# Optimization experiments

Hardware: AMD Instinct MI355X
Metric: run time of the kernel (lower is better)

## Reference

```python
import jax, jax.numpy as jnp
import numpy as np

D_MODEL = 128
N_HEADS = 4
HEAD_DIM = D_MODEL // N_HEADS
NUM_NODES = 64
L = 4096
B = 2


def build_st_causal_mask(seq_len, num_nodes):
    t = seq_len // num_nodes
    time_mask = jnp.tril(jnp.ones((t, t), dtype=bool))  # [T, T]
    # expand to [T, N, T, N] -> [L, L]; attend to all nodes at same/earlier time
    m = jnp.broadcast_to(time_mask[:, None, :, None], (t, num_nodes, t, num_nodes))
    return m.reshape(seq_len, seq_len)


def setup_inputs() -> dict:
    key = jax.random.key(0)
    ks = jax.random.split(key, 12)
    q = jax.random.normal(ks[0], (L, B, D_MODEL), dtype=jnp.float32)
    # xavier-uniform-ish init scales
    lim = np.sqrt(6.0 / (D_MODEL + D_MODEL)) / np.sqrt(2.0)
    W_Q = jax.random.uniform(ks[3], (D_MODEL, D_MODEL), minval=-lim, maxval=lim)
    W_K = jax.random.uniform(ks[4], (D_MODEL, D_MODEL), minval=-lim, maxval=lim)
    W_V = jax.random.uniform(ks[5], (D_MODEL, D_MODEL), minval=-lim, maxval=lim)
    lim_o = np.sqrt(6.0 / (D_MODEL + D_MODEL))
    W_O = jax.random.uniform(ks[6], (D_MODEL, D_MODEL), minval=-lim_o, maxval=lim_o)
    b_Q = jnp.zeros((D_MODEL,), jnp.float32)
    b_K = jnp.zeros((D_MODEL,), jnp.float32)
    b_V = jnp.zeros((D_MODEL,), jnp.float32)
    b_O = jnp.zeros((D_MODEL,), jnp.float32)
    return {
        "query": q,
        "key": jax.random.normal(ks[1], (L, B, D_MODEL), dtype=jnp.float32),
        "value": jax.random.normal(ks[2], (L, B, D_MODEL), dtype=jnp.float32),
        "W_Q": W_Q, "b_Q": b_Q, "W_K": W_K, "b_K": b_K,
        "W_V": W_V, "b_V": b_V, "W_O": W_O, "b_O": b_O,
    }


def reference(query, key, value, W_Q, b_Q, W_K, b_K, W_V, b_V, W_O, b_O):
    Lq, Bq, C = query.shape
    scaling = HEAD_DIM ** (-0.5)
    # torch Linear: x @ W.T + b
    q = (query @ W_Q.T + b_Q) * scaling
    k = key @ W_K.T + b_K
    v = value @ W_V.T + b_V
    # [L, B, C] -> [B, H, L, Dh]
    def split_heads(x):
        return x.reshape(Lq, Bq, N_HEADS, HEAD_DIM).transpose(1, 2, 0, 3)
    q, k, v = split_heads(q), split_heads(k), split_heads(v)
    scores = jnp.einsum("bhqd,bhkd->bhqk", q, k)  # [B, H, L, L]
    mask = build_st_causal_mask(Lq, NUM_NODES)  # [L, L] bool
    scores = jnp.where(mask[None, None], scores, -jnp.inf)
    attn = jax.nn.softmax(scores, axis=-1)
    context = jnp.einsum("bhqk,bhkd->bhqd", attn, v)  # [B, H, L, Dh]
    context = context.transpose(0, 2, 1, 3).reshape(Bq, Lq, C)  # [B, L, C]
    out = context @ W_O.T + b_O  # [B, L, C]
    return out
```

## Files before the change

kernel.cpp:

```cpp
#include <hip/hip_runtime.h>

#define L_SEQ 4096
#define BATCH 2
#define NHEAD 4
#define DHEAD 32
#define DMODEL 128

typedef __attribute__((ext_vector_type(4))) float floatx4;
typedef __attribute__((ext_vector_type(16))) float floatx16;
typedef __attribute__((ext_vector_type(8))) __bf16 bf16x8;
typedef __attribute__((ext_vector_type(8))) unsigned short ushort8;
typedef __attribute__((ext_vector_type(4))) unsigned int uintx4;

__device__ __forceinline__ floatx4 MFMA(ushort8 a, ushort8 b, floatx4 c) {
  return __builtin_amdgcn_mfma_f32_16x16x32_bf16(
      __builtin_bit_cast(bf16x8, a), __builtin_bit_cast(bf16x8, b), c, 0, 0, 0);
}
__device__ __forceinline__ floatx16 MFMA32(ushort8 a, ushort8 b, floatx16 c) {
  return __builtin_amdgcn_mfma_f32_32x32x16_bf16(
      __builtin_bit_cast(bf16x8, a), __builtin_bit_cast(bf16x8, b), c, 0, 0, 0);
}

__device__ __forceinline__ unsigned short f2bf(float f) {
  union { float f; unsigned int u; } x; x.f = f;
  unsigned int u = x.u + 0x7fffu + ((x.u >> 16) & 1u);
  return (unsigned short)(u >> 16);
}

__device__ __forceinline__ unsigned pkbf(float lo, float hi) {
  unsigned r;
  asm("v_cvt_pk_bf16_f32 %0, %1, %2" : "=v"(r) : "v"(lo), "v"(hi));
  return r;
}

#define WLDS 136

__global__ __launch_bounds__(256) void proj_kernel(
    const float* __restrict__ xq, const float* __restrict__ xk,
    const float* __restrict__ xv,
    const float* __restrict__ WQ, const float* __restrict__ bQ,
    const float* __restrict__ WK, const float* __restrict__ bK,
    const float* __restrict__ WV, const float* __restrict__ bV,
    unsigned short* __restrict__ Qs, unsigned short* __restrict__ Ks,
    unsigned short* __restrict__ Vt)
{
  __shared__ unsigned short Wl[128 * WLDS];
  __shared__ float bl[128];
  const int mat = blockIdx.z;
  const int b   = blockIdx.y;
  const int l0  = blockIdx.x * 64;
  const float* __restrict__ x    = (mat == 0) ? xq : (mat == 1) ? xk : xv;
  const float* __restrict__ W    = (mat == 0) ? WQ : (mat == 1) ? WK : WV;
  const float* __restrict__ bias = (mat == 0) ? bQ : (mat == 1) ? bK : bV;
  const int tid = threadIdx.x;

  #pragma unroll
  for (int it = 0; it < 16; ++it) {
    int idx = tid + it * 256;
    int row = idx >> 5;
    int col = (idx & 31) * 4;
    floatx4 v = *(const floatx4*)(W + row * 128 + col);
    unsigned short* dst = Wl + row * WLDS + col;
    dst[0] = f2bf(v[0]); dst[1] = f2bf(v[1]);
    dst[2] = f2bf(v[2]); dst[3] = f2bf(v[3]);
  }
  if (tid < 128) bl[tid] = bias[tid];
  __syncthreads();

  const int w = tid >> 6, lane = tid & 63;
  const int g = lane >> 4, qi = lane & 15;

  ushort8 xf[4];
  #pragma unroll
  for (int kk = 0; kk < 4; ++kk) {
    const float* src = x + ((size_t)(l0 + w * 16 + qi) * BATCH + b) * DMODEL + kk * 32 + g * 8;
    floatx4 a = *(const floatx4*)src;
    floatx4 c = *(const floatx4*)(src + 4);
    ushort8 f;
    f[0]=f2bf(a[0]); f[1]=f2bf(a[1]); f[2]=f2bf(a[2]); f[3]=f2bf(a[3]);
    f[4]=f2bf(c[0]); f[5]=f2bf(c[1]); f[6]=f2bf(c[2]); f[7]=f2bf(c[3]);
    xf[kk] = f;
  }

  floatx4 acc[8];
  #pragma unroll
  for (int n = 0; n < 8; ++n) acc[n] = (floatx4){0.f, 0.f, 0.f, 0.f};

  #pragma unroll
  for (int kk = 0; kk < 4; ++kk) {
    #pragma unroll
    for (int n = 0; n < 8; ++n) {
      ushort8 wf = *(const ushort8*)(Wl + (n * 16 + qi) * WLDS + kk * 32 + g * 8);
      acc[n] = (mat == 2) ? MFMA(wf, xf[kk], acc[n]) : MFMA(xf[kk], wf, acc[n]);
    }
  }

  const int hb4 = b * NHEAD;
  if (mat == 0) {
    const float scale = 0.17677669529663687f;
    #pragma unroll
    for (int n = 0; n < 8; ++n) {
      int c = n * 16 + qi;
      int h = c >> 5, dh = c & 31;
      float bb = bl[c];
      #pragma unroll
      for (int r = 0; r < 4; ++r) {
        int lq = l0 + w * 16 + 4 * g + r;
        float v = (acc[n][r] + bb) * scale;
        Qs[((size_t)(hb4 + h) * L_SEQ + lq) * DHEAD + dh] = f2bf(v);
      }
    }
  } else if (mat == 1) {
    #pragma unroll
    for (int n = 0; n < 8; ++n) {
      int c = n * 16 + qi;
      int h = c >> 5, dh = c & 31;
      int dj  = (dh >> 4) & 1;
      int hi2 = (dh >> 3) & 1;
      int e   = dh & 7;
      float bb = bl[c];
      #pragma unroll
      for (int r = 0; r < 4; ++r) {
        int lq = l0 + w * 16 + 4 * g + r;
        int t   = lq >> 6;
        int rr  = lq & 63;
        int ql2 = rr & 31, rhi = rr >> 5;
        size_t off = ((((size_t)(hb4 + h) * 64 + t) * 4 + (2 * rhi + dj)) * 64
                      + (hi2 * 32 + ql2)) * 8 + e;
        Ks[off] = f2bf(acc[n][r] + bb);
      }
    }
  } else {
    #pragma unroll
    for (int n = 0; n < 8; ++n) {
      #pragma unroll
      for (int r = 0; r < 4; ++r) {
        int cout = n * 16 + 4 * g + r;
        int h = cout >> 5, dh2 = cout & 31;
        float v = acc[n][r] + bl[cout];
        int lq  = l0 + w * 16 + qi;
        int t   = lq >> 6;
        int kvt = lq & 63;
        int s   = kvt >> 4;
        int u   = kvt & 15;
        int b2  = (u >> 3) & 1;
        int hi2 = (u >> 2) & 1;
        int e2  = u & 3;
        size_t off = ((((size_t)(hb4 + h) * 64 + t) * 4 + s) * 64
                      + (hi2 * 32 + dh2)) * 8 + (4 * b2 + e2);
        Vt[off] = f2bf(v);
      }
    }
  }
}

__global__ __launch_bounds__(256, 4) void attn_kernel(
    const unsigned short* __restrict__ Qs, const unsigned short* __restrict__ Ks,
    const unsigned short* __restrict__ Vt,
    float* __restrict__ Opart, float* __restrict__ MLpart)
{
  __shared__ float Tr[4][32 * 36];

  const int tid = threadIdx.x;
  const int w = tid >> 6, lane = tid & 63;
  const int ql = lane & 31, hi = lane >> 5;

  const int ph    = blockIdx.x;
  const int plane = ph >> 1;
  const int half  = ph & 1;
  const int j     = blockIdx.y;
  const int bq    = j & 15, mq = j >> 4;
  const int tq    = (mq == 0) ? bq : (mq == 1) ? 63 - bq
                  : (mq == 2) ? 16 + bq : 47 - bq;

  const int c     = w;
  const int width = (tq >> 2) + 1;
  const int t0    = c * width;
  const int tend  = min(t0 + width, tq + 1);

  const unsigned short* __restrict__ Qh = Qs + (size_t)plane * L_SEQ * DHEAD;

  const int q0 = tq * 64 + half * 32;
  ushort8 qf0 = *(const ushort8*)(Qh + (size_t)(q0 + ql) * DHEAD + hi * 8);
  ushort8 qf1 = *(const ushort8*)(Qh + (size_t)(q0 + ql) * DHEAD + 16 + hi * 8);

  const floatx16 z16 = {0,0,0,0,0,0,0,0,0,0,0,0,0,0,0,0};
  floatx16 acc_a = z16, acc_b = z16;
  float m = -1e30f, l = 0.f;

  const unsigned short* kb = Ks + ((size_t)plane * 64 + t0) * 2048 + (size_t)lane * 8;
  const unsigned short* vb = Vt + ((size_t)plane * 64 + t0) * 2048 + (size_t)lane * 8;

  #pragma unroll 2
  for (int t = t0; t < tend; ++t) {
    ushort8 kf00 = *(const ushort8*)(kb);
    ushort8 kf01 = *(const ushort8*)(kb + 512);
    ushort8 kf10 = *(const ushort8*)(kb + 1024);
    ushort8 kf11 = *(const ushort8*)(kb + 1536);
    ushort8 va0  = *(const ushort8*)(vb);
    ushort8 va1  = *(const ushort8*)(vb + 512);
    ushort8 va2  = *(const ushort8*)(vb + 1024);
    ushort8 va3  = *(const ushort8*)(vb + 1536);
    kb += 2048;
    vb += 2048;

    floatx16 St0 = MFMA32(kf00, qf0, z16);
    St0 = MFMA32(kf01, qf1, St0);
    floatx16 St1 = MFMA32(kf10, qf0, z16);
    St1 = MFMA32(kf11, qf1, St1);

    float pmax = St0[0];
    #pragma unroll
    for (int i = 1; i < 16; ++i) pmax = fmaxf(pmax, St0[i]);
    #pragma unroll
    for (int i = 0; i < 16; ++i) pmax = fmaxf(pmax, St1[i]);
    pmax = fmaxf(pmax, __shfl_xor(pmax, 32));

    if (__any(pmax > m + 8.0f)) {
      float mnew = fmaxf(m, pmax);
      float corr = __expf(m - mnew);
      m = mnew;
      l *= corr;
      #pragma unroll
      for (int i = 0; i < 16; ++i) { acc_a[i] *= corr; acc_b[i] *= corr; }
    }
    float rsum = 0.f;
    #pragma unroll
    for (int i = 0; i < 16; ++i) { float e = __expf(St0[i] - m); St0[i] = e; rsum += e; }
    #pragma unroll
    for (int i = 0; i < 16; ++i) { float e = __expf(St1[i] - m); St1[i] = e; rsum += e; }
    rsum += __shfl_xor(rsum, 32);
    l += rsum;

    uintx4 pb;
    pb[0] = pkbf(St0[0], St0[1]); pb[1] = pkbf(St0[2], St0[3]);
    pb[2] = pkbf(St0[4], St0[5]); pb[3] = pkbf(St0[6], St0[7]);
    acc_a = MFMA32(va0, __builtin_bit_cast(ushort8, pb), acc_a);
    pb[0] = pkbf(St0[8], St0[9]);  pb[1] = pkbf(St0[10], St0[11]);
    pb[2] = pkbf(St0[12], St0[13]); pb[3] = pkbf(St0[14], St0[15]);
    acc_a = MFMA32(va1, __builtin_bit_cast(ushort8, pb), acc_a);
    pb[0] = pkbf(St1[0], St1[1]); pb[1] = pkbf(St1[2], St1[3]);
    pb[2] = pkbf(St1[4], St1[5]); pb[3] = pkbf(St1[6], St1[7]);
    acc_b = MFMA32(va2, __builtin_bit_cast(ushort8, pb), acc_b);
    pb[0] = pkbf(St1[8], St1[9]);  pb[1] = pkbf(St1[10], St1[11]);
    pb[2] = pkbf(St1[12], St1[13]); pb[3] = pkbf(St1[14], St1[15]);
    acc_b = MFMA32(va3, __builtin_bit_cast(ushort8, pb), acc_b);
  }

  const int slot = ((plane * 64 + tq) * 4 + c);
  float* T = &Tr[w][0];
  #pragma unroll
  for (int r = 0; r < 16; ++r) {
    int dh = (r & 3) + 8 * (r >> 2) + 4 * hi;
    T[ql * 36 + dh] = acc_a[r] + acc_b[r];
  }
  asm volatile("s_waitcnt lgkmcnt(0)" ::: "memory");
  __builtin_amdgcn_sched_barrier(0);

  const int qr = lane >> 1, dg = (lane & 1) * 16;
  float* __restrict__ Op = Opart + (size_t)slot * 2048 + half * 32 * 32;
  #pragma unroll
  for (int j2 = 0; j2 < 4; ++j2) {
    floatx4 vv = *(const floatx4*)(T + qr * 36 + dg + 4 * j2);
    *(floatx4*)(Op + qr * 32 + dg + 4 * j2) = vv;
  }
  if (hi == 0) {
    MLpart[(size_t)slot * 128 + (half * 32 + ql) * 2 + 0] = m;
    MLpart[(size_t)slot * 128 + (half * 32 + ql) * 2 + 1] = l;
  }
}

__global__ __launch_bounds__(256) void combine_kernel(
    const float* __restrict__ Opart, const float* __restrict__ MLpart,
    unsigned short* __restrict__ ctx)
{
  const int tq = blockIdx.x;
  const int hb = blockIdx.y;
  const int tid = threadIdx.x;
  const int q  = tid >> 2;
  const int dg = tid & 3;
  const int slot0 = (hb * 64 + tq) * 4;

  float mv[4], lv[4];
  float M = -1e30f;
  #pragma unroll
  for (int ci = 0; ci < 4; ++ci) {
    mv[ci] = MLpart[(size_t)(slot0 + ci) * 128 + q * 2 + 0];
    lv[ci] = MLpart[(size_t)(slot0 + ci) * 128 + q * 2 + 1];
    M = fmaxf(M, mv[ci]);
  }
  float Lsum = 0.f;
  float wgt[4];
  #pragma unroll
  for (int ci = 0; ci < 4; ++ci) {
    wgt[ci] = __expf(mv[ci] - M);
    Lsum += wgt[ci] * lv[ci];
  }
  float inv = 1.0f / Lsum;

  floatx4 a0 = (floatx4){0.f,0.f,0.f,0.f}, a1 = (floatx4){0.f,0.f,0.f,0.f};
  #pragma unroll
  for (int ci = 0; ci < 4; ++ci) {
    const float* Op = Opart + (size_t)(slot0 + ci) * 2048 + q * 32 + dg * 8;
    floatx4 o0 = *(const floatx4*)(Op);
    floatx4 o1 = *(const floatx4*)(Op + 4);
    float wv = wgt[ci];
    a0 += wv * o0;
    a1 += wv * o1;
  }
  const int b = hb >> 2, hh = hb & 3;
  size_t base = ((size_t)b * L_SEQ + tq * 64 + q) * DMODEL + hh * 32 + dg * 8;
  #pragma unroll
  for (int j = 0; j < 4; ++j) {
    ctx[base + j]     = f2bf(a0[j] * inv);
    ctx[base + 4 + j] = f2bf(a1[j] * inv);
  }
}

__global__ __launch_bounds__(256) void oproj_kernel(
    const unsigned short* __restrict__ ctx, const float* __restrict__ WO,
    const float* __restrict__ bO, float* __restrict__ out)
{
  __shared__ unsigned short Wl[64 * WLDS];
  __shared__ float bl[64];
  const int m0 = blockIdx.x * 64;
  const int n0 = blockIdx.y * 64;
  const int tid = threadIdx.x;

  #pragma unroll
  for (int it = 0; it < 8; ++it) {
    int idx = tid + it * 256;
    int row = idx >> 5, col = (idx & 31) * 4;
    floatx4 v = *(const floatx4*)(WO + (size_t)(n0 + row) * 128 + col);
    unsigned short* dst = Wl + row * WLDS + col;
    dst[0] = f2bf(v[0]); dst[1] = f2bf(v[1]);
    dst[2] = f2bf(v[2]); dst[3] = f2bf(v[3]);
  }
  if (tid < 64) bl[tid] = bO[n0 + tid];
  __syncthreads();

  const int w = tid >> 6, lane = tid & 63;
  const int g = lane >> 4, qi = lane & 15;

  ushort8 xf[4];
  #pragma unroll
  for (int kk = 0; kk < 4; ++kk)
    xf[kk] = *(const ushort8*)(ctx + (size_t)(m0 + w * 16 + qi) * DMODEL + kk * 32 + g * 8);

  floatx4 acc[4];
  #pragma unroll
  for (int n = 0; n < 4; ++n) acc[n] = (floatx4){0.f, 0.f, 0.f, 0.f};

  #pragma unroll
  for (int kk = 0; kk < 4; ++kk) {
    #pragma unroll
    for (int n = 0; n < 4; ++n) {
      ushort8 wf = *(const ushort8*)(Wl + (n * 16 + qi) * WLDS + kk * 32 + g * 8);
      acc[n] = MFMA(xf[kk], wf, acc[n]);
    }
  }

  #pragma unroll
  for (int n = 0; n < 4; ++n) {
    int c = n * 16 + qi;
    float bb = bl[c];
    #pragma unroll
    for (int r = 0; r < 4; ++r) {
      int m = m0 + w * 16 + 4 * g + r;
      out[(size_t)m * DMODEL + n0 + c] = acc[n][r] + bb;
    }
  }
}

extern "C" void kernel_launch(void* const* d_in, const int* in_sizes, int n_in,
                              void* d_out, int out_size, void* d_ws, size_t ws_size,
                              hipStream_t stream) {
  const float* q  = (const float*)d_in[0];
  const float* k  = (const float*)d_in[1];
  const float* v  = (const float*)d_in[2];
  const float* WQ = (const float*)d_in[3];
  const float* bQ = (const float*)d_in[4];
  const float* WK = (const float*)d_in[5];
  const float* bK = (const float*)d_in[6];
  const float* WV = (const float*)d_in[7];
  const float* bV = (const float*)d_in[8];
  const float* WO = (const float*)d_in[9];
  const float* bO = (const float*)d_in[10];
  float* out = (float*)d_out;

  const size_t plane = (size_t)BATCH * NHEAD * L_SEQ * DHEAD;
  unsigned short* Qs  = (unsigned short*)d_ws;
  unsigned short* Ks  = Qs + plane;
  unsigned short* Vt  = Ks + plane;
  unsigned short* ctx = Vt + plane;
  float* Opart  = (float*)(ctx + plane);
  float* MLpart = Opart + (size_t)2048 * 2048;

  hipLaunchKernelGGL(proj_kernel, dim3(64, 2, 3), dim3(256), 0, stream,
                     q, k, v, WQ, bQ, WK, bK, WV, bV, Qs, Ks, Vt);
  hipLaunchKernelGGL(attn_kernel, dim3(16, 64), dim3(256), 0, stream,
                     Qs, Ks, Vt, Opart, MLpart);
  hipLaunchKernelGGL(combine_kernel, dim3(64, 8), dim3(256), 0, stream,
                     Opart, MLpart, ctx);
  hipLaunchKernelGGL(oproj_kernel, dim3(128, 2), dim3(256), 0, stream, ctx, WO, bO, out);
}
```

Measured before the change: 41.59 us.

## Fuse split-KV combine into output projection and raise MFMA wave priority

The separate combine kernel is folded into the output-projection kernel. Each block now merges the four partial attention results for all heads of its 64 rows directly into LDS as bf16 context, so the global ctx round-trip and one kernel launch go away. In exchange, both column blocks (n0) redo the same combine work and read Opart twice. The attention inner loop also wraps its MFMA groups in s_setprio to favour matrix issue, and regroups the bf16 packing so two MFMAs issue back to back.

```diff
diff --git a/kernel.cpp b/kernel.cpp
--- a/kernel.cpp
+++ b/kernel.cpp
@@ -204,10 +204,12 @@
     kb += 2048;
     vb += 2048;
 
+    __builtin_amdgcn_s_setprio(1);
     floatx16 St0 = MFMA32(kf00, qf0, z16);
     St0 = MFMA32(kf01, qf1, St0);
     floatx16 St1 = MFMA32(kf10, qf0, z16);
     St1 = MFMA32(kf11, qf1, St1);
+    __builtin_amdgcn_s_setprio(0);
 
     float pmax = St0[0];
     #pragma unroll
@@ -232,19 +234,23 @@
     rsum += __shfl_xor(rsum, 32);
     l += rsum;
 
-    uintx4 pb;
-    pb[0] = pkbf(St0[0], St0[1]); pb[1] = pkbf(St0[2], St0[3]);
-    pb[2] = pkbf(St0[4], St0[5]); pb[3] = pkbf(St0[6], St0[7]);
-    acc_a = MFMA32(va0, __builtin_bit_cast(ushort8, pb), acc_a);
-    pb[0] = pkbf(St0[8], St0[9]);  pb[1] = pkbf(St0[10], St0[11]);
-    pb[2] = pkbf(St0[12], St0[13]); pb[3] = pkbf(St0[14], St0[15]);
-    acc_a = MFMA32(va1, __builtin_bit_cast(ushort8, pb), acc_a);
-    pb[0] = pkbf(St1[0], St1[1]); pb[1] = pkbf(St1[2], St1[3]);
-    pb[2] = pkbf(St1[4], St1[5]); pb[3] = pkbf(St1[6], St1[7]);
-    acc_b = MFMA32(va2, __builtin_bit_cast(ushort8, pb), acc_b);
-    pb[0] = pkbf(St1[8], St1[9]);  pb[1] = pkbf(St1[10], St1[11]);
-    pb[2] = pkbf(St1[12], St1[13]); pb[3] = pkbf(St1[14], St1[15]);
-    acc_b = MFMA32(va3, __builtin_bit_cast(ushort8, pb), acc_b);
+    uintx4 pb0, pb1;
+    pb0[0] = pkbf(St0[0], St0[1]); pb0[1] = pkbf(St0[2], St0[3]);
+    pb0[2] = pkbf(St0[4], St0[5]); pb0[3] = pkbf(St0[6], St0[7]);
+    pb1[0] = pkbf(St0[8], St0[9]);  pb1[1] = pkbf(St0[10], St0[11]);
+    pb1[2] = pkbf(St0[12], St0[13]); pb1[3] = pkbf(St0[14], St0[15]);
+    __builtin_amdgcn_s_setprio(1);
+    acc_a = MFMA32(va0, __builtin_bit_cast(ushort8, pb0), acc_a);
+    acc_a = MFMA32(va1, __builtin_bit_cast(ushort8, pb1), acc_a);
+    __builtin_amdgcn_s_setprio(0);
+    pb0[0] = pkbf(St1[0], St1[1]); pb0[1] = pkbf(St1[2], St1[3]);
+    pb0[2] = pkbf(St1[4], St1[5]); pb0[3] = pkbf(St1[6], St1[7]);
+    pb1[0] = pkbf(St1[8], St1[9]);  pb1[1] = pkbf(St1[10], St1[11]);
+    pb1[2] = pkbf(St1[12], St1[13]); pb1[3] = pkbf(St1[14], St1[15]);
+    __builtin_amdgcn_s_setprio(1);
+    acc_b = MFMA32(va2, __builtin_bit_cast(ushort8, pb0), acc_b);
+    acc_b = MFMA32(va3, __builtin_bit_cast(ushort8, pb1), acc_b);
+    __builtin_amdgcn_s_setprio(0);
   }
 
   const int slot = ((plane * 64 + tq) * 4 + c);
@@ -270,61 +276,18 @@
   }
 }
 
-__global__ __launch_bounds__(256) void combine_kernel(
+__global__ __launch_bounds__(256) void oproj_fused_kernel(
     const float* __restrict__ Opart, const float* __restrict__ MLpart,
-    unsigned short* __restrict__ ctx)
+    const float* __restrict__ WO, const float* __restrict__ bO,
+    float* __restrict__ out)
 {
-  const int tq = blockIdx.x;
-  const int hb = blockIdx.y;
-  const int tid = threadIdx.x;
-  const int q  = tid >> 2;
-  const int dg = tid & 3;
-  const int slot0 = (hb * 64 + tq) * 4;
-
-  float mv[4], lv[4];
-  float M = -1e30f;
-  #pragma unroll
-  for (int ci = 0; ci < 4; ++ci) {
-    mv[ci] = MLpart[(size_t)(slot0 + ci) * 128 + q * 2 + 0];
-    lv[ci] = MLpart[(size_t)(slot0 + ci) * 128 + q * 2 + 1];
-    M = fmaxf(M, mv[ci]);
-  }
-  float Lsum = 0.f;
-  float wgt[4];
-  #pragma unroll
-  for (int ci = 0; ci < 4; ++ci) {
-    wgt[ci] = __expf(mv[ci] - M);
-    Lsum += wgt[ci] * lv[ci];
-  }
-  float inv = 1.0f / Lsum;
-
-  floatx4 a0 = (floatx4){0.f,0.f,0.f,0.f}, a1 = (floatx4){0.f,0.f,0.f,0.f};
-  #pragma unroll
-  for (int ci = 0; ci < 4; ++ci) {
-    const float* Op = Opart + (size_t)(slot0 + ci) * 2048 + q * 32 + dg * 8;
-    floatx4 o0 = *(const floatx4*)(Op);
-    floatx4 o1 = *(const floatx4*)(Op + 4);
-    float wv = wgt[ci];
-    a0 += wv * o0;
-    a1 += wv * o1;
-  }
-  const int b = hb >> 2, hh = hb & 3;
-  size_t base = ((size_t)b * L_SEQ + tq * 64 + q) * DMODEL + hh * 32 + dg * 8;
-  #pragma unroll
-  for (int j = 0; j < 4; ++j) {
-    ctx[base + j]     = f2bf(a0[j] * inv);
-    ctx[base + 4 + j] = f2bf(a1[j] * inv);
-  }
-}
-
-__global__ __launch_bounds__(256) void oproj_kernel(
-    const unsigned short* __restrict__ ctx, const float* __restrict__ WO,
-    const float* __restrict__ bO, float* __restrict__ out)
-{
+  __shared__ unsigned short Cl[64 * WLDS];
   __shared__ unsigned short Wl[64 * WLDS];
   __shared__ float bl[64];
   const int m0 = blockIdx.x * 64;
   const int n0 = blockIdx.y * 64;
+  const int b  = m0 >> 12;
+  const int tq = (m0 >> 6) & 63;
   const int tid = threadIdx.x;
 
   #pragma unroll
@@ -337,6 +300,48 @@
     dst[2] = f2bf(v[2]); dst[3] = f2bf(v[3]);
   }
   if (tid < 64) bl[tid] = bO[n0 + tid];
+
+  {
+    const int q  = tid >> 2;
+    const int dg = tid & 3;
+    #pragma unroll
+    for (int h = 0; h < 4; ++h) {
+      const int slot0 = ((b * 4 + h) * 64 + tq) * 4;
+      float mv[4], lv[4];
+      float M = -1e30f;
+      #pragma unroll
+      for (int ci = 0; ci < 4; ++ci) {
+        mv[ci] = MLpart[(size_t)(slot0 + ci) * 128 + q * 2 + 0];
+        lv[ci] = MLpart[(size_t)(slot0 + ci) * 128 + q * 2 + 1];
+        M = fmaxf(M, mv[ci]);
+      }
+      float Lsum = 0.f;
+      float wgt[4];
+      #pragma unroll
+      for (int ci = 0; ci < 4; ++ci) {
+        wgt[ci] = __expf(mv[ci] - M);
+        Lsum += wgt[ci] * lv[ci];
+      }
+      float inv = 1.0f / Lsum;
+
+      floatx4 a0 = (floatx4){0.f,0.f,0.f,0.f}, a1 = (floatx4){0.f,0.f,0.f,0.f};
+      #pragma unroll
+      for (int ci = 0; ci < 4; ++ci) {
+        const float* Op = Opart + (size_t)(slot0 + ci) * 2048 + q * 32 + dg * 8;
+        floatx4 o0 = *(const floatx4*)(Op);
+        floatx4 o1 = *(const floatx4*)(Op + 4);
+        float wv = wgt[ci];
+        a0 += wv * o0;
+        a1 += wv * o1;
+      }
+      unsigned short* dst = Cl + q * WLDS + h * 32 + dg * 8;
+      #pragma unroll
+      for (int j = 0; j < 4; ++j) {
+        dst[j]     = f2bf(a0[j] * inv);
+        dst[4 + j] = f2bf(a1[j] * inv);
+      }
+    }
+  }
   __syncthreads();
 
   const int w = tid >> 6, lane = tid & 63;
@@ -345,7 +350,7 @@
   ushort8 xf[4];
   #pragma unroll
   for (int kk = 0; kk < 4; ++kk)
-    xf[kk] = *(const ushort8*)(ctx + (size_t)(m0 + w * 16 + qi) * DMODEL + kk * 32 + g * 8);
+    xf[kk] = *(const ushort8*)(Cl + (w * 16 + qi) * WLDS + kk * 32 + g * 8);
 
   floatx4 acc[4];
   #pragma unroll
@@ -366,8 +371,8 @@
     float bb = bl[c];
     #pragma unroll
     for (int r = 0; r < 4; ++r) {
-      int m = m0 + w * 16 + 4 * g + r;
-      out[(size_t)m * DMODEL + n0 + c] = acc[n][r] + bb;
+      int mm = m0 + w * 16 + 4 * g + r;
+      out[(size_t)mm * DMODEL + n0 + c] = acc[n][r] + bb;
     }
   }
 }
@@ -400,7 +405,6 @@
                      q, k, v, WQ, bQ, WK, bK, WV, bV, Qs, Ks, Vt);
   hipLaunchKernelGGL(attn_kernel, dim3(16, 64), dim3(256), 0, stream,
                      Qs, Ks, Vt, Opart, MLpart);
-  hipLaunchKernelGGL(combine_kernel, dim3(64, 8), dim3(256), 0, stream,
-                     Opart, MLpart, ctx);
-  hipLaunchKernelGGL(oproj_kernel, dim3(128, 2), dim3(256), 0, stream, ctx, WO, bO, out);
-}
+  hipLaunchKernelGGL(oproj_fused_kernel, dim3(128, 2), dim3(256), 0, stream,
+                     Opart, MLpart, WO, bO, out);
+}
```

Measured after the change: 39.27 us. 5.6% less time.
